# Performance work log

Measured on AMD Instinct MI355X. Metric: run time of the kernel, lower is better.

The kernel has to match this reference:

```python
import jax, jax.numpy as jnp
import numpy as np

B, T, H = 4, 4096, 1024


def setup_inputs() -> dict:
    key = jax.random.key(0)
    ks = jax.random.split(key, 10)
    W_STD = 0.02  # small init keeps the WKV denominator well-conditioned
    inp = {
        "x": jax.random.normal(ks[0], (B, T, H), dtype=jnp.float32),
        "time_decay": jnp.exp(-jax.random.uniform(ks[1], (H,), minval=0.5, maxval=1.5)),
        "time_mix_key": jax.random.uniform(ks[2], (H,)),
        "time_mix_value": jax.random.uniform(ks[3], (H,)),
        "time_mix_receptance": jax.random.uniform(ks[4], (H,)),
        "W_receptance": jax.random.normal(ks[5], (H, H)) * W_STD,
        "W_key": jax.random.normal(ks[6], (H, H)) * W_STD,
        "W_value": jax.random.normal(ks[7], (H, H)) * W_STD,
        "W_out": jax.random.normal(ks[8], (H, H)) * W_STD,
        "b_out": jax.random.normal(ks[9], (H,)) * W_STD,
    }
    return inp


def reference(x, time_decay, time_mix_key, time_mix_value, time_mix_receptance,
              W_receptance, W_key, W_value, W_out, b_out):
    # time_shift: shifted[:, t] = x[:, t-1], shifted[:, 0] = 0
    shifted = jnp.pad(x, ((0, 0), (1, 0), (0, 0)))[:, :-1]
    xs = x + shifted  # original applies SAME mix to x and shifted
    k = (xs * time_mix_key) @ W_key.T          # [B,T,H]
    v = (xs * time_mix_value) @ W_value.T      # [B,T,H]
    r = jax.nn.sigmoid((xs * time_mix_receptance) @ W_receptance.T)

    def step(carry, kv):
        num, den = carry                       # [B,H] each
        ck, cv = kv                            # [B,H]
        out = (num + time_decay * ck * den) / (den + time_decay * ck)
        ek = jnp.exp(ck)
        return (time_decay * num + ek * cv, time_decay * den + ek), out

    init = (jnp.ones_like(k[:, 0]), jnp.ones_like(k[:, 0]))
    kT = jnp.swapaxes(k, 0, 1)  # [T,B,H]
    vT = jnp.swapaxes(v, 0, 1)
    _, outT = jax.lax.scan(step, init, (kT, vT))
    out = jnp.swapaxes(outT, 0, 1)             # [B,T,H]
    return (r * out) @ W_out.T + b_out
```

## Files before the change

kernel.cpp:

```cpp
#include <hip/hip_runtime.h>

#define H_DIM 1024
#define T_DIM 4096
#define B_DIM 4
#define M_DIM (B_DIM * T_DIM)
#define SCAN_C 64
#define SCAN_W 48

typedef __attribute__((ext_vector_type(8))) short short8;
typedef __attribute__((ext_vector_type(4))) float f32x4;
typedef _Float16 half8 __attribute__((ext_vector_type(8)));

__device__ __forceinline__ unsigned short f2h(float f) {
  _Float16 h = (_Float16)f;
  return __builtin_bit_cast(unsigned short, h);
}
__device__ __forceinline__ float h2f(unsigned short u) {
  return (float)__builtin_bit_cast(_Float16, u);
}

__device__ __forceinline__ double fast_exp64(double x) {
  const double L2E = 1.4426950408889634074;
  const double LN2 = 0.69314718055994530942;
  double z = x * L2E;
  double n = rint(z);
  double y = (z - n) * LN2;
  double p = 2.7557319223985890653e-6;
  p = fma(p, y, 2.4801587301587301566e-5);
  p = fma(p, y, 1.9841269841269841253e-4);
  p = fma(p, y, 1.3888888888888889419e-3);
  p = fma(p, y, 8.3333333333333332177e-3);
  p = fma(p, y, 4.1666666666666664354e-2);
  p = fma(p, y, 1.6666666666666665741e-1);
  p = fma(p, y, 0.5);
  p = fma(p, y, 1.0);
  p = fma(p, y, 1.0);
  long long bits = ((long long)(1023 + (int)n)) << 52;
  return p * __longlong_as_double(bits);
}

__global__ void xs_split_kernel(const float* __restrict__ x,
                                unsigned short* __restrict__ xs1,
                                unsigned short* __restrict__ xs2,
                                int n4) {
  int i = blockIdx.x * blockDim.x + threadIdx.x;
  const int HV = H_DIM / 4;
  if (i >= n4) return;
  int m = i / HV;
  int t = m & (T_DIM - 1);
  float4 cur = reinterpret_cast<const float4*>(x)[i];
  float4 prev = make_float4(0.f, 0.f, 0.f, 0.f);
  if (t > 0) prev = reinterpret_cast<const float4*>(x)[i - HV];
  float s[4] = {cur.x + prev.x, cur.y + prev.y, cur.z + prev.z, cur.w + prev.w};
  unsigned short a1[4], a2[4];
#pragma unroll
  for (int q = 0; q < 4; ++q) {
    unsigned short h1 = f2h(s[q]);
    a1[q] = h1;
    a2[q] = f2h((s[q] - h2f(h1)) * 2048.0f);
  }
  reinterpret_cast<ushort4*>(xs1)[i] = make_ushort4(a1[0], a1[1], a1[2], a1[3]);
  reinterpret_cast<ushort4*>(xs2)[i] = make_ushort4(a2[0], a2[1], a2[2], a2[3]);
}

__global__ void wprep_kernel(const float* __restrict__ Wrec, const float* __restrict__ Wkey,
                             const float* __restrict__ Wval, const float* __restrict__ Wout,
                             const float* __restrict__ tmk, const float* __restrict__ tmv,
                             const float* __restrict__ tmr,
                             unsigned short* __restrict__ WK1H, unsigned short* __restrict__ WK2H,
                             unsigned short* __restrict__ WVRH,
                             unsigned short* __restrict__ WOH) {
  int i = blockIdx.x * blockDim.x + threadIdx.x;
  if (i >= H_DIM * H_DIM) return;
  int j = i & (H_DIM - 1);
  float wk = Wkey[i] * tmk[j];
  unsigned short k1 = f2h(wk);
  WK1H[i] = k1;
  WK2H[i] = f2h((wk - h2f(k1)) * 2048.0f);
  WVRH[i] = f2h(Wval[i] * tmv[j]);
  WVRH[H_DIM * H_DIM + i] = f2h(Wrec[i] * tmr[j]);
  WOH[i] = f2h(Wout[i]);
}

#define GBAR() do { asm volatile("" ::: "memory"); __builtin_amdgcn_sched_barrier(0); \
                    __builtin_amdgcn_s_barrier(); \
                    __builtin_amdgcn_sched_barrier(0); asm volatile("" ::: "memory"); } while (0)
#define WAIT_VM6() asm volatile("s_waitcnt vmcnt(6)" ::: "memory")
#define WAIT_VM0() asm volatile("s_waitcnt vmcnt(0)" ::: "memory")

__device__ __forceinline__ f32x4 mma_h(short8 a, short8 b, f32x4 c) {
  return __builtin_amdgcn_mfma_f32_16x16x32_f16(
      __builtin_bit_cast(half8, a), __builtin_bit_cast(half8, b), c, 0, 0, 0);
}
__device__ __forceinline__ f32x4 mma_hh(half8 a, short8 b, f32x4 c) {
  return __builtin_amdgcn_mfma_f32_16x16x32_f16(a, __builtin_bit_cast(half8, b), c, 0, 0, 0);
}

__device__ __forceinline__ void stage_r128(const unsigned short* base, int rowoff, int kt,
                                           unsigned dst, int wid, int lane,
                                           unsigned char* smem) {
  int row = wid * 16 + (lane >> 2);
  int col8 = (lane & 3) ^ ((row >> 1) & 3);
  const unsigned short* src = base + (size_t)(rowoff + row) * 1024 + kt * 32 + col8 * 8;
  __builtin_amdgcn_global_load_lds(
      (const __attribute__((address_space(1))) void*)src,
      (__attribute__((address_space(3))) void*)(smem + dst + wid * 1024), 16, 0, 0);
}
__device__ __forceinline__ void stage_r256(const unsigned short* base, int rowoff, int kt,
                                           unsigned dst, int wid, int lane,
                                           unsigned char* smem) {
#pragma unroll
  for (int i = 0; i < 2; ++i) {
    int row = wid * 32 + i * 16 + (lane >> 2);
    int col8 = (lane & 3) ^ ((row >> 1) & 3);
    const unsigned short* src = base + (size_t)(rowoff + row) * 1024 + kt * 32 + col8 * 8;
    __builtin_amdgcn_global_load_lds(
        (const __attribute__((address_space(1))) void*)src,
        (__attribute__((address_space(3))) void*)(smem + dst + wid * 2048 + i * 1024), 16, 0, 0);
  }
}
__device__ __forceinline__ short8 frag_ld2(const unsigned char* smem, unsigned rbase,
                                           int row, int kg) {
  return *reinterpret_cast<const short8*>(smem + rbase + row * 64 + ((kg ^ ((row >> 1) & 3)) * 16));
}

__device__ void gemm_k_body(const unsigned short* __restrict__ A1,
                            const unsigned short* __restrict__ A2,
                            const unsigned short* __restrict__ B1,
                            const unsigned short* __restrict__ B2,
                            float* __restrict__ C, int bid, unsigned char* smem) {
  const int tid = threadIdx.x;
  const int wid = tid >> 6;
  const int lane = tid & 63;
  const int wm = wid >> 2;
  const int wn = wid & 3;
  const int frow = lane & 15;
  const int kg = lane >> 4;
  const int swz = (bid & 7) * 64 + (bid >> 3);
  const int brow = (swz >> 2) << 7;
  const int bcol = (swz & 3) << 8;

  f32x4 acc0[4][4], acc1[4][4];
#pragma unroll
  for (int f = 0; f < 4; ++f)
#pragma unroll
    for (int c = 0; c < 4; ++c) {
      acc0[f][c] = (f32x4){0.f, 0.f, 0.f, 0.f};
      acc1[f][c] = (f32x4){0.f, 0.f, 0.f, 0.f};
    }

  const int NT = 32;
#pragma unroll
  for (int t0 = 0; t0 < 2; ++t0) {
    unsigned sb = t0 * 49152u;
    stage_r128(A1, brow, t0, sb + 0u, wid, lane, smem);
    stage_r128(A2, brow, t0, sb + 8192u, wid, lane, smem);
    stage_r256(B1, bcol, t0, sb + 16384u, wid, lane, smem);
    stage_r256(B2, bcol, t0, sb + 32768u, wid, lane, smem);
  }
  WAIT_VM6();
  GBAR();

  for (int t = 0; t < NT; ++t) {
    unsigned sb = (unsigned)(t % 3) * 49152u;
    unsigned st = (unsigned)((t + 2) % 3) * 49152u;
    const bool stg = (t + 2 < NT);
    short8 a1[4], a2[4], b1[4], b2[4];
#pragma unroll
    for (int f = 0; f < 4; ++f) a1[f] = frag_ld2(smem, sb + 0u, wm * 64 + f * 16 + frow, kg);
#pragma unroll
    for (int c = 0; c < 4; ++c) b1[c] = frag_ld2(smem, sb + 16384u, wn * 64 + c * 16 + frow, kg);
#pragma unroll
    for (int c = 0; c < 4; ++c) b2[c] = frag_ld2(smem, sb + 32768u, wn * 64 + c * 16 + frow, kg);
    if (stg) {
      stage_r128(A1, brow, t + 2, st + 0u, wid, lane, smem);
      stage_r128(A2, brow, t + 2, st + 8192u, wid, lane, smem);
    }
    GBAR();
    __builtin_amdgcn_s_setprio(1);
#pragma unroll
    for (int f = 0; f < 4; ++f)
#pragma unroll
      for (int c = 0; c < 4; ++c)
        acc0[f][c] = mma_h(a1[f], b1[c], acc0[f][c]);
#pragma unroll
    for (int f = 0; f < 4; ++f)
#pragma unroll
      for (int c = 0; c < 4; ++c)
        acc1[f][c] = mma_h(a1[f], b2[c], acc1[f][c]);
    __builtin_amdgcn_s_setprio(0);
    GBAR();
#pragma unroll
    for (int f = 0; f < 4; ++f) a2[f] = frag_ld2(smem, sb + 8192u, wm * 64 + f * 16 + frow, kg);
    if (stg) {
      stage_r256(B1, bcol, t + 2, st + 16384u, wid, lane, smem);
      stage_r256(B2, bcol, t + 2, st + 32768u, wid, lane, smem);
    }
    WAIT_VM6();
    GBAR();
    __builtin_amdgcn_s_setprio(1);
#pragma unroll
    for (int f = 0; f < 4; ++f)
#pragma unroll
      for (int c = 0; c < 4; ++c)
        acc1[f][c] = mma_h(a2[f], b1[c], acc1[f][c]);
#pragma unroll
    for (int f = 0; f < 4; ++f) {
      half8 ad = __builtin_bit_cast(half8, a2[f]) * (_Float16)0.00048828125f;
#pragma unroll
      for (int c = 0; c < 4; ++c)
        acc1[f][c] = mma_hh(ad, b2[c], acc1[f][c]);
    }
    __builtin_amdgcn_s_setprio(0);
    GBAR();
  }
  WAIT_VM0();

#pragma unroll
  for (int f = 0; f < 4; ++f) {
    int r0 = brow + wm * 64 + f * 16 + kg * 4;
#pragma unroll
    for (int c = 0; c < 4; ++c) {
      int cc = bcol + wn * 64 + c * 16 + frow;
#pragma unroll
      for (int q = 0; q < 4; ++q)
        C[(size_t)(r0 + q) * H_DIM + cc] =
            fmaf(0.00048828125f, acc1[f][c][q], acc0[f][c][q]);
    }
  }
}

__device__ __forceinline__ void stage_half(const unsigned short* base, int rowoff,
                                           int ktp, int kk, int slot,
                                           int wid, int lane, unsigned char* smem) {
#pragma unroll
  for (int i = 0; i < 2; ++i) {
    int row = wid * 32 + i * 16 + (lane >> 2);
    int kcol8 = (lane & 3) ^ ((row >> 1) & 3);
    const unsigned short* src = base + (size_t)(rowoff + row) * 1024
                                + ktp * 64 + kk * 32 + kcol8 * 8;
    unsigned int doff = (unsigned int)(slot * 16384 + wid * 2048 + i * 1024);
    __builtin_amdgcn_global_load_lds(
        (const __attribute__((address_space(1))) void*)src,
        (__attribute__((address_space(3))) void*)(smem + doff), 16, 0, 0);
  }
}
__device__ __forceinline__ short8 frag_ld(const unsigned char* smem, int slot, int row, int kg) {
  int byte = slot * 16384 + row * 64 + ((kg ^ ((row >> 1) & 3)) * 16);
  return *reinterpret_cast<const short8*>(smem + byte);
}

__device__ void gemm_vr_body(const unsigned short* __restrict__ Ag,
                             const unsigned short* __restrict__ Bg,
                             unsigned short* __restrict__ C, int bid,
                             unsigned char* smem) {
  const int tid = threadIdx.x;
  const int wid = tid >> 6;
  const int lane = tid & 63;
  const int wm = wid >> 2;
  const int wn = wid & 3;
  const int frow = lane & 15;
  const int kg = lane >> 4;
  const int swz = (bid & 7) * 64 + (bid >> 3);
  const int brow = (swz >> 3) << 8;
  const int bcol = (swz & 7) << 8;

  f32x4 acc[8][4];
#pragma unroll
  for (int f = 0; f < 8; ++f)
#pragma unroll
    for (int c = 0; c < 4; ++c)
      acc[f][c] = (f32x4){0.f, 0.f, 0.f, 0.f};

  const int NT = 16;
  stage_half(Ag, brow, 0, 0, 0, wid, lane, smem);
  stage_half(Bg, bcol, 0, 0, 1, wid, lane, smem);
  stage_half(Ag, brow, 0, 1, 2, wid, lane, smem);
  stage_half(Bg, bcol, 0, 1, 3, wid, lane, smem);
  stage_half(Ag, brow, 1, 0, 4, wid, lane, smem);
  stage_half(Bg, bcol, 1, 0, 5, wid, lane, smem);
  stage_half(Ag, brow, 1, 1, 6, wid, lane, smem);
  WAIT_VM6();
  GBAR();

  for (int t = 0; t < NT; ++t) {
    const int cur4 = (t & 1) * 4;
    const int nxt4 = cur4 ^ 4;
    short8 a[4], b[4];
#pragma unroll
    for (int f = 0; f < 4; ++f) a[f] = frag_ld(smem, cur4 + 0, wm * 128 + f * 16 + frow, kg);
#pragma unroll
    for (int c = 0; c < 4; ++c) b[c] = frag_ld(smem, cur4 + 1, wn * 64 + c * 16 + frow, kg);
    if (t + 1 < NT) stage_half(Bg, bcol, t + 1, 1, nxt4 + 3, wid, lane, smem);
    GBAR();
    __builtin_amdgcn_s_setprio(1);
#pragma unroll
    for (int f = 0; f < 4; ++f)
#pragma unroll
      for (int c = 0; c < 4; ++c)
        acc[f][c] = mma_h(a[f], b[c], acc[f][c]);
    __builtin_amdgcn_s_setprio(0);
    GBAR();
#pragma unroll
    for (int f = 0; f < 4; ++f) a[f] = frag_ld(smem, cur4 + 0, wm * 128 + (f + 4) * 16 + frow, kg);
    if (t + 2 < NT) stage_half(Ag, brow, t + 2, 0, cur4 + 0, wid, lane, smem);
    GBAR();
    __builtin_amdgcn_s_setprio(1);
#pragma unroll
    for (int f = 0; f < 4; ++f)
#pragma unroll
      for (int c = 0; c < 4; ++c)
        acc[f + 4][c] = mma_h(a[f], b[c], acc[f + 4][c]);
    __builtin_amdgcn_s_setprio(0);
    GBAR();
#pragma unroll
    for (int f = 0; f < 4; ++f) a[f] = frag_ld(smem, cur4 + 2, wm * 128 + f * 16 + frow, kg);
#pragma unroll
    for (int c = 0; c < 4; ++c) b[c] = frag_ld(smem, cur4 + 3, wn * 64 + c * 16 + frow, kg);
    if (t + 2 < NT) stage_half(Bg, bcol, t + 2, 0, cur4 + 1, wid, lane, smem);
    GBAR();
    __builtin_amdgcn_s_setprio(1);
#pragma unroll
    for (int f = 0; f < 4; ++f)
#pragma unroll
      for (int c = 0; c < 4; ++c)
        acc[f][c] = mma_h(a[f], b[c], acc[f][c]);
    __builtin_amdgcn_s_setprio(0);
    GBAR();
#pragma unroll
    for (int f = 0; f < 4; ++f) a[f] = frag_ld(smem, cur4 + 2, wm * 128 + (f + 4) * 16 + frow, kg);
    if (t + 2 < NT) stage_half(Ag, brow, t + 2, 1, cur4 + 2, wid, lane, smem);
    WAIT_VM6();
    GBAR();
    __builtin_amdgcn_s_setprio(1);
#pragma unroll
    for (int f = 0; f < 4; ++f)
#pragma unroll
      for (int c = 0; c < 4; ++c)
        acc[f + 4][c] = mma_h(a[f], b[c], acc[f + 4][c]);
    __builtin_amdgcn_s_setprio(0);
    GBAR();
  }
  WAIT_VM0();

#pragma unroll
  for (int f = 0; f < 8; ++f) {
    int r0 = brow + wm * 128 + f * 16 + kg * 4;
#pragma unroll
    for (int c = 0; c < 4; ++c) {
      int cc = bcol + wn * 64 + c * 16 + frow;
#pragma unroll
      for (int q = 0; q < 4; ++q)
        C[(size_t)(r0 + q) * 2048 + cc] = f2h(acc[f][c][q]);
    }
  }
}

__global__ __launch_bounds__(512, 2) void front_kernel(
    const unsigned short* __restrict__ XS1, const unsigned short* __restrict__ XS2,
    const unsigned short* __restrict__ WK1, const unsigned short* __restrict__ WK2,
    const unsigned short* __restrict__ WVR,
    float* __restrict__ Ck, unsigned short* __restrict__ Cvr) {
  __shared__ __attribute__((aligned(16))) unsigned char smem[147456];
  int bid = blockIdx.x;
  if (bid < 512)
    gemm_k_body(XS1, XS2, WK1, WK2, Ck, bid, smem);
  else
    gemm_vr_body(XS1, WVR, Cvr, bid - 512, smem);
}

__global__ __launch_bounds__(512, 2) void gemm_o_kernel(const unsigned short* __restrict__ Ag,
                                                        const unsigned short* __restrict__ Bg,
                                                        float* __restrict__ C,
                                                        const float* __restrict__ bias) {
  __shared__ __attribute__((aligned(16))) unsigned char smem[131072];
  const int tid = threadIdx.x;
  const int wid = tid >> 6;
  const int lane = tid & 63;
  const int wm = wid >> 2;
  const int wn = wid & 3;
  const int frow = lane & 15;
  const int kg = lane >> 4;
  const int nwg = gridDim.x * gridDim.y;
  const int wg = blockIdx.y * gridDim.x + blockIdx.x;
  const int swz = (wg & 7) * (nwg >> 3) + (wg >> 3);
  const int brow = (swz / gridDim.x) << 8;
  const int bcol = (swz % gridDim.x) << 8;

  f32x4 acc[8][4];
#pragma unroll
  for (int f = 0; f < 8; ++f)
#pragma unroll
    for (int c = 0; c < 4; ++c)
      acc[f][c] = (f32x4){0.f, 0.f, 0.f, 0.f};

  const int NT = 16;
  stage_half(Ag, brow, 0, 0, 0, wid, lane, smem);
  stage_half(Bg, bcol, 0, 0, 1, wid, lane, smem);
  stage_half(Ag, brow, 0, 1, 2, wid, lane, smem);
  stage_half(Bg, bcol, 0, 1, 3, wid, lane, smem);
  stage_half(Ag, brow, 1, 0, 4, wid, lane, smem);
  stage_half(Bg, bcol, 1, 0, 5, wid, lane, smem);
  stage_half(Ag, brow, 1, 1, 6, wid, lane, smem);
  WAIT_VM6();
  GBAR();

  for (int t = 0; t < NT; ++t) {
    const int cur4 = (t & 1) * 4;
    const int nxt4 = cur4 ^ 4;
    short8 a[4], b[4];
#pragma unroll
    for (int f = 0; f < 4; ++f) a[f] = frag_ld(smem, cur4 + 0, wm * 128 + f * 16 + frow, kg);
#pragma unroll
    for (int c = 0; c < 4; ++c) b[c] = frag_ld(smem, cur4 + 1, wn * 64 + c * 16 + frow, kg);
    if (t + 1 < NT) stage_half(Bg, bcol, t + 1, 1, nxt4 + 3, wid, lane, smem);
    GBAR();
    __builtin_amdgcn_s_setprio(1);
#pragma unroll
    for (int f = 0; f < 4; ++f)
#pragma unroll
      for (int c = 0; c < 4; ++c)
        acc[f][c] = mma_h(a[f], b[c], acc[f][c]);
    __builtin_amdgcn_s_setprio(0);
    GBAR();
#pragma unroll
    for (int f = 0; f < 4; ++f) a[f] = frag_ld(smem, cur4 + 0, wm * 128 + (f + 4) * 16 + frow, kg);
    if (t + 2 < NT) stage_half(Ag, brow, t + 2, 0, cur4 + 0, wid, lane, smem);
    GBAR();
    __builtin_amdgcn_s_setprio(1);
#pragma unroll
    for (int f = 0; f < 4; ++f)
#pragma unroll
      for (int c = 0; c < 4; ++c)
        acc[f + 4][c] = mma_h(a[f], b[c], acc[f + 4][c]);
    __builtin_amdgcn_s_setprio(0);
    GBAR();
#pragma unroll
    for (int f = 0; f < 4; ++f) a[f] = frag_ld(smem, cur4 + 2, wm * 128 + f * 16 + frow, kg);
#pragma unroll
    for (int c = 0; c < 4; ++c) b[c] = frag_ld(smem, cur4 + 3, wn * 64 + c * 16 + frow, kg);
    if (t + 2 < NT) stage_half(Bg, bcol, t + 2, 0, cur4 + 1, wid, lane, smem);
    GBAR();
    __builtin_amdgcn_s_setprio(1);
#pragma unroll
    for (int f = 0; f < 4; ++f)
#pragma unroll
      for (int c = 0; c < 4; ++c)
        acc[f][c] = mma_h(a[f], b[c], acc[f][c]);
    __builtin_amdgcn_s_setprio(0);
    GBAR();
#pragma unroll
    for (int f = 0; f < 4; ++f) a[f] = frag_ld(smem, cur4 + 2, wm * 128 + (f + 4) * 16 + frow, kg);
    if (t + 2 < NT) stage_half(Ag, brow, t + 2, 1, cur4 + 2, wid, lane, smem);
    WAIT_VM6();
    GBAR();
    __builtin_amdgcn_s_setprio(1);
#pragma unroll
    for (int f = 0; f < 4; ++f)
#pragma unroll
      for (int c = 0; c < 4; ++c)
        acc[f + 4][c] = mma_h(a[f], b[c], acc[f + 4][c]);
    __builtin_amdgcn_s_setprio(0);
    GBAR();
  }
  WAIT_VM0();

#pragma unroll
  for (int f = 0; f < 8; ++f) {
    int r0 = brow + wm * 128 + f * 16 + kg * 4;
#pragma unroll
    for (int c = 0; c < 4; ++c) {
      int cc = bcol + wn * 64 + c * 16 + frow;
      float bb = bias[cc];
#pragma unroll
      for (int q = 0; q < 4; ++q)
        C[(size_t)(r0 + q) * H_DIM + cc] = acc[f][c][q] + bb;
    }
  }
}

__global__ void wkv_scan_kernel(const float* __restrict__ kbuf,
                                const unsigned short* __restrict__ vrbuf,
                                const float* __restrict__ tdec,
                                unsigned short* __restrict__ rwh) {
  const int h = blockIdx.x * 64 + threadIdx.x;
  const int chunk = blockIdx.y;
  const int b = blockIdx.z;
  const int t0 = chunk * SCAN_C;
  const int tstart = (chunk == 0) ? 0 : (t0 - SCAN_W);
  const int tend = t0 + SCAN_C;
  double num, den;
  if (chunk == 0) { num = 1.0; den = 1.0; } else { num = 0.0; den = 0.0; }
  const double w = (double)tdec[h];
  size_t ik = ((size_t)b * T_DIM + tstart) * H_DIM + h;
  size_t iv = ((size_t)b * T_DIM + tstart) * 2048 + h;
  float kc = kbuf[ik];
  unsigned short vc = vrbuf[iv];
  unsigned short rc = vrbuf[iv + 1024];
  for (int t = tstart; t < tend; ++t) {
    int adv = (t + 1 < tend) ? 1 : 0;
    float kn = kbuf[ik + adv * H_DIM];
    unsigned short vn = vrbuf[iv + adv * 2048];
    unsigned short rn = vrbuf[iv + adv * 2048 + 1024];
    double ck = (double)kc;
    if (t >= t0) {
      double p = w * ck;
      double A = fma(p, den, num);
      double Bd = den + p;
      float outf = (float)A / (float)Bd;
      float rr = 1.0f / (1.0f + __expf(-h2f(rc)));
      rwh[ik] = f2h(rr * outf);
    }
    double ek = fast_exp64(ck);
    num = fma(w, num, ek * (double)h2f(vc));
    den = fma(w, den, ek);
    kc = kn; vc = vn; rc = rn;
    ik += H_DIM; iv += 2048;
  }
}

extern "C" void kernel_launch(void* const* d_in, const int* in_sizes, int n_in,
                              void* d_out, int out_size, void* d_ws, size_t ws_size,
                              hipStream_t stream) {
  const float* x    = (const float*)d_in[0];
  const float* tdec = (const float*)d_in[1];
  const float* tmk  = (const float*)d_in[2];
  const float* tmv  = (const float*)d_in[3];
  const float* tmr  = (const float*)d_in[4];
  const float* Wrec = (const float*)d_in[5];
  const float* Wkey = (const float*)d_in[6];
  const float* Wval = (const float*)d_in[7];
  const float* Wout = (const float*)d_in[8];
  const float* bout = (const float*)d_in[9];
  float* out = (float*)d_out;
  unsigned char* ws = (unsigned char*)d_ws;

  const size_t W2 = (size_t)H_DIM * H_DIM * 2;
  const size_t BF_FULL = (size_t)M_DIM * H_DIM * 2;
  const size_t NEED = 2 * BF_FULL + 2 * BF_FULL + 5 * W2;
  if (ws_size < NEED) return;

  size_t off = 0;
  unsigned short* XS1H = (unsigned short*)(ws + off); off += BF_FULL;
  unsigned short* XS2H = (unsigned short*)(ws + off); off += BF_FULL;
  unsigned short* VR   = (unsigned short*)(ws + off); off += 2 * BF_FULL;
  unsigned short* WK1H = (unsigned short*)(ws + off); off += W2;
  unsigned short* WK2H = (unsigned short*)(ws + off); off += W2;
  unsigned short* WVRH = (unsigned short*)(ws + off); off += 2 * W2;
  unsigned short* WOH  = (unsigned short*)(ws + off); off += W2;

  wprep_kernel<<<dim3(H_DIM * H_DIM / 256), dim3(256), 0, stream>>>(
      Wrec, Wkey, Wval, Wout, tmk, tmv, tmr, WK1H, WK2H, WVRH, WOH);

  int n4 = M_DIM * (H_DIM / 4);
  xs_split_kernel<<<dim3(n4 / 256), dim3(256), 0, stream>>>(x, XS1H, XS2H, n4);

  front_kernel<<<dim3(1024), dim3(512), 0, stream>>>(
      XS1H, XS2H, WK1H, WK2H, WVRH, out, VR);

  unsigned short* RWH = XS1H;
  wkv_scan_kernel<<<dim3(H_DIM / 64, T_DIM / SCAN_C, B_DIM), dim3(64), 0, stream>>>(
      out, VR, tdec, RWH);

  gemm_o_kernel<<<dim3(H_DIM / 256, M_DIM / 256), dim3(512), 0, stream>>>(
      RWH, WOH, out, bout);
}
```

Before: 322.2 us.

## Merge prep kernels, drop key-GEMM correction term, pair channels in scan

Fuses the activation-split and weight-prep kernels into one launch, using block-index ranges to pick which job each block does. Removes the fourth split-precision MFMA term (xs residual times WK residual) from the key GEMM, which cuts matrix work per k-step. Also makes each scan thread process two adjacent channels with vectorized loads and stores, halving the scan grid. Dropping the residual-residual product slightly lowers key precision, and the scan now has fewer threads in flight.

```diff
diff --git a/kernel.cpp b/kernel.cpp
--- a/kernel.cpp
+++ b/kernel.cpp
@@ -39,47 +39,44 @@
   return p * __longlong_as_double(bits);
 }
 
-__global__ void xs_split_kernel(const float* __restrict__ x,
-                                unsigned short* __restrict__ xs1,
-                                unsigned short* __restrict__ xs2,
-                                int n4) {
-  int i = blockIdx.x * blockDim.x + threadIdx.x;
-  const int HV = H_DIM / 4;
-  if (i >= n4) return;
-  int m = i / HV;
-  int t = m & (T_DIM - 1);
-  float4 cur = reinterpret_cast<const float4*>(x)[i];
-  float4 prev = make_float4(0.f, 0.f, 0.f, 0.f);
-  if (t > 0) prev = reinterpret_cast<const float4*>(x)[i - HV];
-  float s[4] = {cur.x + prev.x, cur.y + prev.y, cur.z + prev.z, cur.w + prev.w};
-  unsigned short a1[4], a2[4];
-#pragma unroll
-  for (int q = 0; q < 4; ++q) {
-    unsigned short h1 = f2h(s[q]);
-    a1[q] = h1;
-    a2[q] = f2h((s[q] - h2f(h1)) * 2048.0f);
-  }
-  reinterpret_cast<ushort4*>(xs1)[i] = make_ushort4(a1[0], a1[1], a1[2], a1[3]);
-  reinterpret_cast<ushort4*>(xs2)[i] = make_ushort4(a2[0], a2[1], a2[2], a2[3]);
-}
-
-__global__ void wprep_kernel(const float* __restrict__ Wrec, const float* __restrict__ Wkey,
-                             const float* __restrict__ Wval, const float* __restrict__ Wout,
-                             const float* __restrict__ tmk, const float* __restrict__ tmv,
-                             const float* __restrict__ tmr,
-                             unsigned short* __restrict__ WK1H, unsigned short* __restrict__ WK2H,
-                             unsigned short* __restrict__ WVRH,
-                             unsigned short* __restrict__ WOH) {
-  int i = blockIdx.x * blockDim.x + threadIdx.x;
-  if (i >= H_DIM * H_DIM) return;
-  int j = i & (H_DIM - 1);
-  float wk = Wkey[i] * tmk[j];
-  unsigned short k1 = f2h(wk);
-  WK1H[i] = k1;
-  WK2H[i] = f2h((wk - h2f(k1)) * 2048.0f);
-  WVRH[i] = f2h(Wval[i] * tmv[j]);
-  WVRH[H_DIM * H_DIM + i] = f2h(Wrec[i] * tmr[j]);
-  WOH[i] = f2h(Wout[i]);
+__global__ void prep_kernel(const float* __restrict__ x,
+                            const float* __restrict__ Wrec, const float* __restrict__ Wkey,
+                            const float* __restrict__ Wval, const float* __restrict__ Wout,
+                            const float* __restrict__ tmk, const float* __restrict__ tmv,
+                            const float* __restrict__ tmr,
+                            unsigned short* __restrict__ xs1, unsigned short* __restrict__ xs2,
+                            unsigned short* __restrict__ WK1H, unsigned short* __restrict__ WK2H,
+                            unsigned short* __restrict__ WVRH, unsigned short* __restrict__ WOH) {
+  int bid = blockIdx.x;
+  if (bid < 16384) {
+    int i = bid * 256 + threadIdx.x;
+    const int HV = H_DIM / 4;
+    int m = i / HV;
+    int t = m & (T_DIM - 1);
+    float4 cur = reinterpret_cast<const float4*>(x)[i];
+    float4 prev = make_float4(0.f, 0.f, 0.f, 0.f);
+    if (t > 0) prev = reinterpret_cast<const float4*>(x)[i - HV];
+    float s[4] = {cur.x + prev.x, cur.y + prev.y, cur.z + prev.z, cur.w + prev.w};
+    unsigned short a1[4], a2[4];
+#pragma unroll
+    for (int q = 0; q < 4; ++q) {
+      unsigned short h1 = f2h(s[q]);
+      a1[q] = h1;
+      a2[q] = f2h((s[q] - h2f(h1)) * 2048.0f);
+    }
+    reinterpret_cast<ushort4*>(xs1)[i] = make_ushort4(a1[0], a1[1], a1[2], a1[3]);
+    reinterpret_cast<ushort4*>(xs2)[i] = make_ushort4(a2[0], a2[1], a2[2], a2[3]);
+  } else {
+    int i = (bid - 16384) * 256 + threadIdx.x;
+    int j = i & (H_DIM - 1);
+    float wk = Wkey[i] * tmk[j];
+    unsigned short k1 = f2h(wk);
+    WK1H[i] = k1;
+    WK2H[i] = f2h((wk - h2f(k1)) * 2048.0f);
+    WVRH[i] = f2h(Wval[i] * tmv[j]);
+    WVRH[H_DIM * H_DIM + i] = f2h(Wrec[i] * tmr[j]);
+    WOH[i] = f2h(Wout[i]);
+  }
 }
 
 #define GBAR() do { asm volatile("" ::: "memory"); __builtin_amdgcn_sched_barrier(0); \
@@ -91,9 +88,6 @@
 __device__ __forceinline__ f32x4 mma_h(short8 a, short8 b, f32x4 c) {
   return __builtin_amdgcn_mfma_f32_16x16x32_f16(
       __builtin_bit_cast(half8, a), __builtin_bit_cast(half8, b), c, 0, 0, 0);
-}
-__device__ __forceinline__ f32x4 mma_hh(half8 a, short8 b, f32x4 c) {
-  return __builtin_amdgcn_mfma_f32_16x16x32_f16(a, __builtin_bit_cast(half8, b), c, 0, 0, 0);
 }
 
 __device__ __forceinline__ void stage_r128(const unsigned short* base, int rowoff, int kt,
@@ -204,13 +198,6 @@
 #pragma unroll
       for (int c = 0; c < 4; ++c)
         acc1[f][c] = mma_h(a2[f], b1[c], acc1[f][c]);
-#pragma unroll
-    for (int f = 0; f < 4; ++f) {
-      half8 ad = __builtin_bit_cast(half8, a2[f]) * (_Float16)0.00048828125f;
-#pragma unroll
-      for (int c = 0; c < 4; ++c)
-        acc1[f][c] = mma_hh(ad, b2[c], acc1[f][c]);
-    }
     __builtin_amdgcn_s_setprio(0);
     GBAR();
   }
@@ -483,37 +470,43 @@
                                 const unsigned short* __restrict__ vrbuf,
                                 const float* __restrict__ tdec,
                                 unsigned short* __restrict__ rwh) {
-  const int h = blockIdx.x * 64 + threadIdx.x;
+  const int h = (blockIdx.x * 64 + threadIdx.x) * 2;
   const int chunk = blockIdx.y;
   const int b = blockIdx.z;
   const int t0 = chunk * SCAN_C;
   const int tstart = (chunk == 0) ? 0 : (t0 - SCAN_W);
   const int tend = t0 + SCAN_C;
-  double num, den;
-  if (chunk == 0) { num = 1.0; den = 1.0; } else { num = 0.0; den = 0.0; }
-  const double w = (double)tdec[h];
+  double num0, den0, num1, den1;
+  if (chunk == 0) { num0 = num1 = 1.0; den0 = den1 = 1.0; }
+  else            { num0 = num1 = 0.0; den0 = den1 = 0.0; }
+  const double w0 = (double)tdec[h];
+  const double w1 = (double)tdec[h + 1];
   size_t ik = ((size_t)b * T_DIM + tstart) * H_DIM + h;
   size_t iv = ((size_t)b * T_DIM + tstart) * 2048 + h;
-  float kc = kbuf[ik];
-  unsigned short vc = vrbuf[iv];
-  unsigned short rc = vrbuf[iv + 1024];
+  float2 kc = *reinterpret_cast<const float2*>(kbuf + ik);
+  unsigned int vc = *reinterpret_cast<const unsigned int*>(vrbuf + iv);
+  unsigned int rc = *reinterpret_cast<const unsigned int*>(vrbuf + iv + 1024);
   for (int t = tstart; t < tend; ++t) {
-    int adv = (t + 1 < tend) ? 1 : 0;
-    float kn = kbuf[ik + adv * H_DIM];
-    unsigned short vn = vrbuf[iv + adv * 2048];
-    unsigned short rn = vrbuf[iv + adv * 2048 + 1024];
-    double ck = (double)kc;
+    size_t adv = (t + 1 < tend) ? 1 : 0;
+    float2 kn = *reinterpret_cast<const float2*>(kbuf + ik + adv * H_DIM);
+    unsigned int vn = *reinterpret_cast<const unsigned int*>(vrbuf + iv + adv * 2048);
+    unsigned int rn = *reinterpret_cast<const unsigned int*>(vrbuf + iv + adv * 2048 + 1024);
+    double ck0 = (double)kc.x, ck1 = (double)kc.y;
     if (t >= t0) {
-      double p = w * ck;
-      double A = fma(p, den, num);
-      double Bd = den + p;
-      float outf = (float)A / (float)Bd;
-      float rr = 1.0f / (1.0f + __expf(-h2f(rc)));
-      rwh[ik] = f2h(rr * outf);
-    }
-    double ek = fast_exp64(ck);
-    num = fma(w, num, ek * (double)h2f(vc));
-    den = fma(w, den, ek);
+      double p0 = w0 * ck0, p1 = w1 * ck1;
+      float o0 = (float)fma(p0, den0, num0) / (float)(den0 + p0);
+      float o1 = (float)fma(p1, den1, num1) / (float)(den1 + p1);
+      float rr0 = 1.0f / (1.0f + __expf(-h2f((unsigned short)(rc & 0xffffu))));
+      float rr1 = 1.0f / (1.0f + __expf(-h2f((unsigned short)(rc >> 16))));
+      unsigned int wout = (unsigned int)f2h(rr0 * o0) | ((unsigned int)f2h(rr1 * o1) << 16);
+      *reinterpret_cast<unsigned int*>(rwh + ik) = wout;
+    }
+    double ek0 = fast_exp64(ck0);
+    double ek1 = fast_exp64(ck1);
+    num0 = fma(w0, num0, ek0 * (double)h2f((unsigned short)(vc & 0xffffu)));
+    den0 = fma(w0, den0, ek0);
+    num1 = fma(w1, num1, ek1 * (double)h2f((unsigned short)(vc >> 16)));
+    den1 = fma(w1, den1, ek1);
     kc = kn; vc = vn; rc = rn;
     ik += H_DIM; iv += 2048;
   }
@@ -549,17 +542,14 @@
   unsigned short* WVRH = (unsigned short*)(ws + off); off += 2 * W2;
   unsigned short* WOH  = (unsigned short*)(ws + off); off += W2;
 
-  wprep_kernel<<<dim3(H_DIM * H_DIM / 256), dim3(256), 0, stream>>>(
-      Wrec, Wkey, Wval, Wout, tmk, tmv, tmr, WK1H, WK2H, WVRH, WOH);
-
-  int n4 = M_DIM * (H_DIM / 4);
-  xs_split_kernel<<<dim3(n4 / 256), dim3(256), 0, stream>>>(x, XS1H, XS2H, n4);
+  prep_kernel<<<dim3(16384 + 4096), dim3(256), 0, stream>>>(
+      x, Wrec, Wkey, Wval, Wout, tmk, tmv, tmr, XS1H, XS2H, WK1H, WK2H, WVRH, WOH);
 
   front_kernel<<<dim3(1024), dim3(512), 0, stream>>>(
       XS1H, XS2H, WK1H, WK2H, WVRH, out, VR);
 
   unsigned short* RWH = XS1H;
-  wkv_scan_kernel<<<dim3(H_DIM / 64, T_DIM / SCAN_C, B_DIM), dim3(64), 0, stream>>>(
+  wkv_scan_kernel<<<dim3(H_DIM / 128, T_DIM / SCAN_C, B_DIM), dim3(64), 0, stream>>>(
       out, VR, tdec, RWH);
 
   gemm_o_kernel<<<dim3(H_DIM / 256, M_DIM / 256), dim3(512), 0, stream>>>(
```

Result: faster. 303.5 us (-5.8%).
